# Optimization experiments

Hardware: AMD Instinct MI355X
Metric: run time of the kernel (lower is better)

Reference implementation:

```python
import jax, jax.numpy as jnp
import numpy as np

N, E = 20000, 160000          # nodes, edges
D, ED, H, NH = 32, 16, 64, 4  # node_dim, edge_dim, hidden_dim, num_heads
G, MAXN = 100, 200            # graphs, nodes per graph (equal-size graphs)
HD = H // NH                  # head dim


def setup_inputs() -> dict:
    key = jax.random.key(0)
    ks = jax.random.split(key, 20)
    p = lambda k, shp: jax.random.normal(k, shp, dtype=jnp.float32) * 0.05
    return {
        "x": jax.random.normal(ks[0], (N, D), dtype=jnp.float32),
        "edge_index": jax.random.randint(ks[1], (2, E), 0, N),
        "edge_attr": jax.random.normal(ks[2], (E, ED), dtype=jnp.float32),
        "batch": jnp.arange(N, dtype=jnp.int32) // MAXN,  # 100 graphs x 200 nodes
        "en_w1": p(ks[3], (H, ED)), "en_b1": p(ks[4], (H,)),
        "en_w2": p(ks[5], (D * H, H)), "en_b2": p(ks[6], (D * H,)),
        "root_w": p(ks[7], (D, H)), "conv_b": p(ks[8], (H,)),
        "in_proj_w": p(ks[9], (3 * H, H)), "in_proj_b": p(ks[10], (3 * H,)),
        "out_proj_w": p(ks[11], (H, H)), "out_proj_b": p(ks[12], (H,)),
        "lin1_w": p(ks[13], (H, H)), "lin1_b": p(ks[14], (H,)),
        "lin2_w": p(ks[15], (1, H)), "lin2_b": p(ks[16], (1,)),
    }


def reference(x, edge_index, edge_attr, batch,
              en_w1, en_b1, en_w2, en_b2, root_w, conv_b,
              in_proj_w, in_proj_b, out_proj_w, out_proj_b,
              lin1_w, lin1_b, lin2_w, lin2_b):
    src, dst = edge_index[0], edge_index[1]
    # ---- NNConv: edge MLP -> per-edge weight [E, D, H], gather-matmul-scatter-mean ----
    h = jax.nn.relu(edge_attr @ en_w1.T + en_b1)
    w_e = (h @ en_w2.T + en_b2).reshape(E, D, H)
    msgs = jnp.einsum('ed,edh->eh', x[src], w_e)                 # [E, H]
    agg = jax.ops.segment_sum(msgs, dst, num_segments=N)         # scatter-sum by dest
    cnt = jax.ops.segment_sum(jnp.ones((E,), x.dtype), dst, num_segments=N)
    agg = agg / jnp.maximum(cnt, 1.0)[:, None]                   # mean aggregation
    xh = jax.nn.relu(agg + x @ root_w + conv_b)                  # root weight + bias
    # ---- to_dense_batch (batch is sorted) ----
    counts = jax.ops.segment_sum(jnp.ones((N,), jnp.int32), batch, num_segments=G)
    starts = jnp.concatenate([jnp.zeros((1,), jnp.int32), jnp.cumsum(counts)[:-1]])
    pos = jnp.arange(N, dtype=jnp.int32) - starts[batch]
    dense = jnp.zeros((G, MAXN, H), xh.dtype).at[batch, pos].set(xh)
    mask = jnp.zeros((G, MAXN), bool).at[batch, pos].set(True)
    # ---- MultiheadAttention (self-attn, key_padding_mask = ~mask) ----
    qkv = dense @ in_proj_w.T + in_proj_b                        # [G, MAXN, 3H]
    q, k, v = jnp.split(qkv, 3, axis=-1)
    sh = lambda t: t.reshape(G, MAXN, NH, HD).transpose(0, 2, 1, 3)  # [G, NH, MAXN, HD]
    q, k, v = sh(q), sh(k), sh(v)
    scores = jnp.einsum('gnqd,gnkd->gnqk', q, k) / jnp.sqrt(jnp.float32(HD))
    scores = jnp.where(mask[:, None, None, :], scores, jnp.float32(-1e9))
    attn = jax.nn.softmax(scores, axis=-1)
    ctx = jnp.einsum('gnqk,gnkd->gnqd', attn, v)
    ctx = ctx.transpose(0, 2, 1, 3).reshape(G, MAXN, H)
    attn_out = ctx @ out_proj_w.T + out_proj_b
    # zero out padded positions, masked mean pool
    attn_out = jnp.where(mask[:, :, None], attn_out, 0.0)
    graph_emb = attn_out.sum(axis=1) / mask.sum(axis=1, keepdims=True).astype(attn_out.dtype)
    h1 = jax.nn.relu(graph_emb @ lin1_w.T + lin1_b)
    return (h1 @ lin2_w.T + lin2_b).squeeze(1)                   # [G]
```

## Files before the change

kernel.cpp:

```cpp
#include <hip/hip_runtime.h>
#include <math.h>

#define N_N 20000
#define N_E 160000
#define KA 2112
#define NKB 66

typedef __attribute__((ext_vector_type(8))) short bfrag;
typedef __attribute__((ext_vector_type(4))) float facc;

__device__ __forceinline__ unsigned short f2bf(float f) {
  union { float f; unsigned u; } v; v.f = f;
  unsigned u = v.u;
  return (unsigned short)((u + 0x7FFF + ((u >> 16) & 1)) >> 16);
}
__device__ __forceinline__ unsigned pk2(float a, float b) {
  return (unsigned)f2bf(a) | ((unsigned)f2bf(b) << 16);
}
__device__ __forceinline__ float bflo(unsigned u) {
  union { unsigned u; float f; } v; v.u = u << 16; return v.f;
}
__device__ __forceinline__ float bfhi(unsigned u) {
  union { unsigned u; float f; } v; v.u = u & 0xffff0000u; return v.f;
}
__device__ __forceinline__ void gload16(const void* g, void* s) {
  __builtin_amdgcn_global_load_lds(
      (const __attribute__((address_space(1))) void*)g,
      (__attribute__((address_space(3))) void*)s, 16, 0, 0);
}

__global__ __launch_bounds__(256) void k_mlp1(const float* __restrict__ ea,
    const float* __restrict__ w1, const float* __restrict__ b1,
    const int* __restrict__ elist, unsigned short* __restrict__ hes) {
  int t = threadIdx.x, w = t >> 6, j = t & 63;
  int p0 = blockIdx.x * 32 + w * 8;
  float wr[16];
#pragma unroll
  for (int i = 0; i < 16; ++i) wr[i] = w1[j * 16 + i];
  float bj = b1[j];
#pragma unroll
  for (int q = 0; q < 8; ++q) {
    int p = p0 + q;
    int e = elist[p];
    const float* a = ea + (size_t)e * 16;
    float s = bj;
#pragma unroll
    for (int i = 0; i < 16; ++i) s += a[i] * wr[i];
    hes[(size_t)p * 64 + j] = f2bf(fmaxf(s, 0.f));
  }
}

__global__ __launch_bounds__(256) void k_hist(const int* __restrict__ eidx,
    int* __restrict__ cnt) {
  int e = blockIdx.x * 256 + threadIdx.x;
  atomicAdd(&cnt[eidx[N_E + e]], 1);
}

__global__ __launch_bounds__(1024) void k_scan(int* __restrict__ hist,
    int* __restrict__ starts) {
  __shared__ int part[1024];
  int t = threadIdx.x;
  const int CH = 20;
  int lo = t * CH;
  int hi = lo + CH; if (hi > N_N) hi = N_N;
  int s = 0;
  for (int i = lo; i < hi; ++i) s += hist[i];
  part[t] = s;
  __syncthreads();
  for (int off = 1; off < 1024; off <<= 1) {
    int v = (t >= off) ? part[t - off] : 0;
    __syncthreads();
    part[t] += v;
    __syncthreads();
  }
  int run = (t == 0) ? 0 : part[t - 1];
  for (int i = lo; i < hi; ++i) {
    int h = hist[i];
    starts[i] = run;
    hist[i] = run;
    run += h;
  }
  if (t == 1023) starts[N_N] = part[1023];
}

__global__ __launch_bounds__(256) void k_scatter(const int* __restrict__ eidx,
    int* __restrict__ cur, int* __restrict__ elist, int* __restrict__ srcl) {
  int e = blockIdx.x * 256 + threadIdx.x;
  int dn = eidx[N_E + e];
  int pos = atomicAdd(&cur[dn], 1);
  elist[pos] = e;
  srcl[pos] = eidx[e];
}

__global__ __launch_bounds__(256) void k_pack(const float* __restrict__ w2,
    const float* __restrict__ b2f, const float* __restrict__ rootw,
    const float* __restrict__ inw,
    unsigned short* __restrict__ Bp, unsigned short* __restrict__ B2p,
    int* __restrict__ cursor, float* __restrict__ pool) {
  int idx = blockIdx.x * 256 + threadIdx.x;
  const int GT = 580 * 256;
  if (idx < 135168) {
    int i = idx & 7, l = (idx >> 3) & 63, cbkb = idx >> 9;
    int cb = cbkb & 3, kb = cbkb >> 2;
    int r = kb * 32 + ((l >> 4) << 3) + i;
    int c = (cb << 4) + (l & 15);
    float v;
    if (r < 2048) { int d = r >> 6, k = r & 63; v = w2[((d << 6) + c) * 64 + k]; }
    else if (r < 2080) v = b2f[((r - 2048) << 6) + c];
    else v = rootw[((r - 2080) << 6) + c];
    Bp[idx] = f2bf(v);
  } else if (idx < 135168 + 12288) {
    int k2 = idx - 135168;
    int i = k2 & 7, l = (k2 >> 3) & 63, cbkb = k2 >> 9;
    int cb = cbkb % 12, kb = cbkb / 12;
    int r = kb * 32 + ((l >> 4) << 3) + i;
    int c = (cb << 4) + (l & 15);
    B2p[k2] = f2bf(inw[c * 64 + r]);
  }
  for (int i = idx; i < N_N; i += GT) cursor[i] = 0;
  for (int i = idx; i < 6400; i += GT) pool[i] = 0.f;
}

#define FMA8(hv, base, xv) \
  acc[base + 0] += xv * bflo(hv.x); acc[base + 1] += xv * bfhi(hv.x); \
  acc[base + 2] += xv * bflo(hv.y); acc[base + 3] += xv * bfhi(hv.y); \
  acc[base + 4] += xv * bflo(hv.z); acc[base + 5] += xv * bfhi(hv.z); \
  acc[base + 6] += xv * bflo(hv.w); acc[base + 7] += xv * bfhi(hv.w);

__global__ __launch_bounds__(512, 4) void k_fused(const float* __restrict__ x,
    const unsigned short* __restrict__ hes, const int* __restrict__ starts,
    const int* __restrict__ srcl,
    const unsigned short* __restrict__ Bp, const unsigned short* __restrict__ B2p,
    const float* __restrict__ convb, const float* __restrict__ inb,
    float* __restrict__ Qb, float* __restrict__ Kb, float* __restrict__ Vb) {
  __shared__ unsigned short Ps[8 * KA];
  __shared__ __align__(16) unsigned short Hs[8 * 512];
  __shared__ __align__(16) float Xs[8 * 256];
  __shared__ unsigned short xhT[8 * 68];
  int t = threadIdx.x, w = t >> 6, l = t & 63;
  int n0 = blockIdx.x * 8;
  int d0 = l >> 3, l31 = l & 31;
  unsigned short* Hw = Hs + w * 512;
  float* Xw = Xs + w * 256;
  {
    int n = n0 + w;
    int s0 = starts[n], s1 = starts[n + 1];
    float acc[32];
#pragma unroll
    for (int z = 0; z < 32; ++z) acc[z] = 0.f;
    float xs = 0.f;
#pragma unroll 1
    for (int c0 = s0; c0 < s1; c0 += 64) {
      int srv = 0;
      if (c0 + l < s1) srv = srcl[c0 + l];
      int cc = s1 - c0; if (cc > 64) cc = 64;
#pragma unroll 1
      for (int j0 = 0; j0 < cc; j0 += 8) {
        int nedge = cc - j0; if (nedge > 8) nedge = 8;
        int slot = c0 + j0 + (l >> 3); if (slot >= s1) slot = s1 - 1;
        gload16(hes + (size_t)slot * 64 + (l & 7) * 8, Hw);
        int sr = __shfl(srv, j0 + (l >> 3));
        gload16(x + (size_t)sr * 32 + (l & 7) * 4, Xw);
        asm volatile("s_waitcnt vmcnt(0)" ::: "memory");
#pragma unroll 1
        for (int i = 0; i < nedge; i += 2) {
          uint4 hA = *(const uint4*)(Hw + i * 64 + (l & 7) * 8);
          float a0 = Xw[i * 32 + d0],      a1 = Xw[i * 32 + d0 + 8];
          float a2 = Xw[i * 32 + d0 + 16], a3 = Xw[i * 32 + d0 + 24];
          float xsa = Xw[i * 32 + l31];
          uint4 hB = {0, 0, 0, 0};
          float b0 = 0.f, b1 = 0.f, b2 = 0.f, b3 = 0.f, xsb = 0.f;
          if (i + 1 < nedge) {
            hB = *(const uint4*)(Hw + (i + 1) * 64 + (l & 7) * 8);
            b0 = Xw[(i + 1) * 32 + d0];      b1 = Xw[(i + 1) * 32 + d0 + 8];
            b2 = Xw[(i + 1) * 32 + d0 + 16]; b3 = Xw[(i + 1) * 32 + d0 + 24];
            xsb = Xw[(i + 1) * 32 + l31];
          }
          FMA8(hA, 0, a0) FMA8(hA, 8, a1) FMA8(hA, 16, a2) FMA8(hA, 24, a3)
          FMA8(hB, 0, b0) FMA8(hB, 8, b1) FMA8(hB, 16, b2) FMA8(hB, 24, b3)
          xs += xsa + xsb;
        }
      }
    }
    int s = w;
#pragma unroll
    for (int q = 0; q < 4; ++q) {
      int scr = (l + 64 * q) ^ s;
      uint4 o;
      o.x = pk2(acc[q * 8 + 0], acc[q * 8 + 1]);
      o.y = pk2(acc[q * 8 + 2], acc[q * 8 + 3]);
      o.z = pk2(acc[q * 8 + 4], acc[q * 8 + 5]);
      o.w = pk2(acc[q * 8 + 6], acc[q * 8 + 7]);
      *(uint4*)(Ps + w * KA + scr * 8) = o;
    }
    if (l < 32) {
      int cnt = s1 - s0; if (cnt < 1) cnt = 1;
      int c1 = (256 + (l >> 3)) ^ s, c2 = (260 + (l >> 3)) ^ s;
      Ps[w * KA + c1 * 8 + (l & 7)] = f2bf(xs);
      Ps[w * KA + c2 * 8 + (l & 7)] = f2bf(x[(size_t)n * 32 + l] * (float)cnt);
    }
  }
  __syncthreads();
  int col = l & 15, sub = l >> 4;
  int arow = col & 7;
  if (w < 4) {
    const bfrag* Bb = (const bfrag*)Bp + w * 64 + l;
    facc ac = {0.f, 0.f, 0.f, 0.f};
#pragma unroll 4
    for (int kb = 0; kb < NKB; ++kb) {
      int scr = ((kb << 2) + sub) ^ arow;
      bfrag af = *(const bfrag*)(Ps + arow * KA + scr * 8);
      ac = __builtin_amdgcn_mfma_f32_16x16x32_bf16(af, Bb[kb * 256], ac, 0, 0, 0);
    }
    float cv = convb[w * 16 + col];
#pragma unroll
    for (int j = 0; j < 4; ++j) {
      int m = sub * 4 + j;
      if (m < 8) {
        int n = n0 + m;
        int cnt = starts[n + 1] - starts[n]; if (cnt < 1) cnt = 1;
        float inv = 1.f / (float)cnt;
        xhT[m * 68 + w * 16 + col] = f2bf(fmaxf(ac[j] * inv + cv, 0.f));
      }
    }
  }
  __syncthreads();
  if (w < 4) {
    bfrag af0 = *(const bfrag*)&xhT[(col & 7) * 68 + sub * 8];
    bfrag af1 = *(const bfrag*)&xhT[(col & 7) * 68 + 32 + sub * 8];
    const bfrag* B2b = (const bfrag*)B2p + l;
#pragma unroll
    for (int c3 = 0; c3 < 3; ++c3) {
      int cb = w * 3 + c3;
      facc qa = {0.f, 0.f, 0.f, 0.f};
      qa = __builtin_amdgcn_mfma_f32_16x16x32_bf16(af0, B2b[cb * 64], qa, 0, 0, 0);
      qa = __builtin_amdgcn_mfma_f32_16x16x32_bf16(af1, B2b[(12 + cb) * 64], qa, 0, 0, 0);
#pragma unroll
      for (int j = 0; j < 4; ++j) {
        int m = sub * 4 + j;
        if (m < 8) {
          int n = n0 + m;
          int g = n / 200, p = n - g * 200;
          int c = cb * 16 + col;
          float v = qa[j] + inb[c];
          int part = c >> 6, rem = c & 63, hh = rem >> 4, dd = rem & 15;
          float* dst = (part == 0) ? Qb : (part == 1 ? Kb : Vb);
          dst[(((size_t)g * 4 + hh) * 200 + p) * 16 + dd] = v;
        }
      }
    }
  }
}

__global__ __launch_bounds__(256) void k_attn(const float* __restrict__ Qb,
    const float* __restrict__ Kb, const float* __restrict__ Vb,
    float* __restrict__ pool) {
  __shared__ unsigned short Ks[224 * 24];
  __shared__ unsigned short Vt[16 * 232];
  __shared__ unsigned short Pl[4][16 * 40];
  __shared__ float pw[4][16];
  int t = threadIdx.x;
  int gh = blockIdx.x >> 1, half = blockIdx.x & 1;
  size_t base = (size_t)gh * 3200;
  for (int idx = t; idx < 224 * 16; idx += 256) {
    int row = idx >> 4, d = idx & 15;
    float kv = (row < 200) ? Kb[base + idx] : 0.f;
    float vv = (row < 200) ? Vb[base + idx] : 0.f;
    Ks[row * 24 + d] = f2bf(kv);
    Vt[d * 232 + row] = f2bf(vv);
  }
  __syncthreads();
  int w = t >> 6, l = t & 63;
  int sub = l >> 4, col = l & 15;
  int qlo = half * 7, qhi = half ? 13 : 7;
  float pacc = 0.f;
  for (int qt = qlo + w; qt < qhi; qt += 4) {
    bfrag qf = {0, 0, 0, 0, 0, 0, 0, 0};
    int q = qt * 16 + col;
    if (sub < 2 && q < 200) {
      const float* qp = Qb + base + q * 16 + sub * 8;
      float4 qa = *(const float4*)qp;
      float4 qb = *(const float4*)(qp + 4);
      qf[0] = (short)f2bf(qa.x); qf[1] = (short)f2bf(qa.y);
      qf[2] = (short)f2bf(qa.z); qf[3] = (short)f2bf(qa.w);
      qf[4] = (short)f2bf(qb.x); qf[5] = (short)f2bf(qb.y);
      qf[6] = (short)f2bf(qb.z); qf[7] = (short)f2bf(qb.w);
    }
    facc o = {0.f, 0.f, 0.f, 0.f};
    float srow0 = 0.f, srow1 = 0.f, srow2 = 0.f, srow3 = 0.f;
    for (int kt2 = 0; kt2 < 7; ++kt2) {
      int kt0 = kt2 * 2, kt1 = kt0 + 1;
      bfrag kf0 = {0, 0, 0, 0, 0, 0, 0, 0};
      bfrag kf1 = {0, 0, 0, 0, 0, 0, 0, 0};
      if (sub < 2) {
        kf0 = *(const bfrag*)&Ks[(kt0 * 16 + col) * 24 + sub * 8];
        kf1 = *(const bfrag*)&Ks[(kt1 * 16 + col) * 24 + sub * 8];
      }
      facc z = {0.f, 0.f, 0.f, 0.f};
      facc s0 = __builtin_amdgcn_mfma_f32_16x16x32_bf16(qf, kf0, z, 0, 0, 0);
      facc s1 = __builtin_amdgcn_mfma_f32_16x16x32_bf16(qf, kf1, z, 0, 0, 0);
      bool ok0 = (kt0 * 16 + col) < 200;
      bool ok1 = (kt1 * 16 + col) < 200;
#pragma unroll
      for (int j = 0; j < 4; ++j) {
        float e0 = ok0 ? __expf(s0[j] * 0.25f) : 0.f;
        float e1 = ok1 ? __expf(s1[j] * 0.25f) : 0.f;
        if (j == 0) { srow0 += e0 + e1; } else if (j == 1) { srow1 += e0 + e1; }
        else if (j == 2) { srow2 += e0 + e1; } else { srow3 += e0 + e1; }
        int qr = (sub << 2) + j;
        Pl[w][qr * 40 + col] = f2bf(e0);
        Pl[w][qr * 40 + 16 + col] = f2bf(e1);
      }
      bfrag pf = *(const bfrag*)&Pl[w][col * 40 + sub * 8];
      bfrag vf = *(const bfrag*)&Vt[col * 232 + kt2 * 32 + sub * 8];
      o = __builtin_amdgcn_mfma_f32_16x16x32_bf16(pf, vf, o, 0, 0, 0);
    }
#pragma unroll
    for (int off = 1; off < 16; off <<= 1) {
      srow0 += __shfl_xor(srow0, off);
      srow1 += __shfl_xor(srow1, off);
      srow2 += __shfl_xor(srow2, off);
      srow3 += __shfl_xor(srow3, off);
    }
#pragma unroll
    for (int j = 0; j < 4; ++j) {
      int qq = qt * 16 + (sub << 2) + j;
      float sr = (j == 0) ? srow0 : (j == 1) ? srow1 : (j == 2) ? srow2 : srow3;
      if (qq < 200) pacc += o[j] / sr;
    }
  }
  pacc += __shfl_xor(pacc, 16);
  pacc += __shfl_xor(pacc, 32);
  if (l < 16) pw[w][l] = pacc;
  __syncthreads();
  if (t < 16) {
    float v = pw[0][t] + pw[1][t] + pw[2][t] + pw[3][t];
    atomicAdd(&pool[gh * 16 + t], v);
  }
}

__global__ __launch_bounds__(64) void k_head(const float* __restrict__ pool,
    const float* __restrict__ ow, const float* __restrict__ ob,
    const float* __restrict__ w1, const float* __restrict__ b1,
    const float* __restrict__ w2, const float* __restrict__ b2,
    float* __restrict__ out) {
  __shared__ float ms[64], es[64];
  int g = blockIdx.x, t = threadIdx.x;
  ms[t] = pool[g * 64 + t] * (1.f / 200.f);
  __syncthreads();
  float e = ob[t];
  for (int j = 0; j < 64; ++j) e += ow[t * 64 + j] * ms[j];
  es[t] = e;
  __syncthreads();
  float h1 = b1[t];
  for (int j = 0; j < 64; ++j) h1 += w1[t * 64 + j] * es[j];
  h1 = fmaxf(h1, 0.f);
  float pr = h1 * w2[t];
  for (int off = 32; off >= 1; off >>= 1) pr += __shfl_xor(pr, off);
  if (t == 0) out[g] = pr + b2[0];
}

extern "C" void kernel_launch(void* const* d_in, const int* in_sizes, int n_in,
                              void* d_out, int out_size, void* d_ws, size_t ws_size,
                              hipStream_t stream) {
  (void)in_sizes; (void)n_in;
  const float* x      = (const float*)d_in[0];
  const int*   eidx   = (const int*)d_in[1];
  const float* ea     = (const float*)d_in[2];
  const float* en_w1  = (const float*)d_in[4];
  const float* en_b1  = (const float*)d_in[5];
  const float* en_w2  = (const float*)d_in[6];
  const float* en_b2  = (const float*)d_in[7];
  const float* root_w = (const float*)d_in[8];
  const float* conv_b = (const float*)d_in[9];
  const float* in_w   = (const float*)d_in[10];
  const float* in_b   = (const float*)d_in[11];
  const float* out_w  = (const float*)d_in[12];
  const float* out_b  = (const float*)d_in[13];
  const float* l1w    = (const float*)d_in[14];
  const float* l1b    = (const float*)d_in[15];
  const float* l2w    = (const float*)d_in[16];
  const float* l2b    = (const float*)d_in[17];
  float* out = (float*)d_out;

  char* w = (char*)d_ws;
  unsigned short* hes = (unsigned short*)w;
  float* Qb  = (float*)(w + 20480000);
  float* Kb  = (float*)(w + 25600000);
  float* Vb  = (float*)(w + 30720000);
  float* pool = (float*)(w + 35840000);
  char* r3 = w + 35870000;
  unsigned short* Bp  = (unsigned short*)r3;
  unsigned short* B2p = (unsigned short*)(r3 + 270336);
  int* starts = (int*)(r3 + 270336 + 24576);
  int* elist  = starts + (N_N + 4);
  int* srcl   = elist + N_E;
  int* cursor = srcl + N_E;
  size_t need = 35870000 + 270336 + 24576
              + (size_t)(N_N + 4) * 4 + 2 * (size_t)N_E * 4 + (size_t)N_N * 4;
  if (ws_size < need || out_size < 100) return;

  k_pack<<<580, 256, 0, stream>>>(en_w2, en_b2, root_w, in_w, Bp, B2p, cursor, pool);
  k_hist<<<N_E / 256, 256, 0, stream>>>(eidx, cursor);
  k_scan<<<1, 1024, 0, stream>>>(cursor, starts);
  k_scatter<<<N_E / 256, 256, 0, stream>>>(eidx, cursor, elist, srcl);
  k_mlp1<<<5000, 256, 0, stream>>>(ea, en_w1, en_b1, elist, hes);
  k_fused<<<2500, 512, 0, stream>>>(x, hes, starts, srcl, Bp, B2p,
                                    conv_b, in_b, Qb, Kb, Vb);
  k_attn<<<800, 256, 0, stream>>>(Qb, Kb, Vb, pool);
  k_head<<<100, 64, 0, stream>>>(pool, out_w, out_b, l1w, l1b, l2w, l2b, out);
}
```

Baseline: 165.3 us.

## Fuse edge MLP into message kernel, merge histogram into pack, fold head into attention

The first edge-MLP layer (edge_attr -> 64 hidden ReLU) moves into the fused message kernel. Each wave loads raw 16-float edge attributes and computes the bf16 hidden activations in LDS, so the 20 MB intermediate no longer makes a global round trip. The destination histogram now runs inside the weight-packing kernel, with a memset zeroing the cursor first. The final MLP head is folded into the attention kernel through a last-block-done atomic counter per graph. Together these remove three launches at the cost of some extra ALU work per edge chunk and a serialized tail in the last block for each graph.

```diff
diff --git a/kernel.cpp b/kernel.cpp
--- a/kernel.cpp
+++ b/kernel.cpp
@@ -29,76 +29,12 @@
       (__attribute__((address_space(3))) void*)s, 16, 0, 0);
 }
 
-__global__ __launch_bounds__(256) void k_mlp1(const float* __restrict__ ea,
-    const float* __restrict__ w1, const float* __restrict__ b1,
-    const int* __restrict__ elist, unsigned short* __restrict__ hes) {
-  int t = threadIdx.x, w = t >> 6, j = t & 63;
-  int p0 = blockIdx.x * 32 + w * 8;
-  float wr[16];
-#pragma unroll
-  for (int i = 0; i < 16; ++i) wr[i] = w1[j * 16 + i];
-  float bj = b1[j];
-#pragma unroll
-  for (int q = 0; q < 8; ++q) {
-    int p = p0 + q;
-    int e = elist[p];
-    const float* a = ea + (size_t)e * 16;
-    float s = bj;
-#pragma unroll
-    for (int i = 0; i < 16; ++i) s += a[i] * wr[i];
-    hes[(size_t)p * 64 + j] = f2bf(fmaxf(s, 0.f));
-  }
-}
-
-__global__ __launch_bounds__(256) void k_hist(const int* __restrict__ eidx,
-    int* __restrict__ cnt) {
-  int e = blockIdx.x * 256 + threadIdx.x;
-  atomicAdd(&cnt[eidx[N_E + e]], 1);
-}
-
-__global__ __launch_bounds__(1024) void k_scan(int* __restrict__ hist,
-    int* __restrict__ starts) {
-  __shared__ int part[1024];
-  int t = threadIdx.x;
-  const int CH = 20;
-  int lo = t * CH;
-  int hi = lo + CH; if (hi > N_N) hi = N_N;
-  int s = 0;
-  for (int i = lo; i < hi; ++i) s += hist[i];
-  part[t] = s;
-  __syncthreads();
-  for (int off = 1; off < 1024; off <<= 1) {
-    int v = (t >= off) ? part[t - off] : 0;
-    __syncthreads();
-    part[t] += v;
-    __syncthreads();
-  }
-  int run = (t == 0) ? 0 : part[t - 1];
-  for (int i = lo; i < hi; ++i) {
-    int h = hist[i];
-    starts[i] = run;
-    hist[i] = run;
-    run += h;
-  }
-  if (t == 1023) starts[N_N] = part[1023];
-}
-
-__global__ __launch_bounds__(256) void k_scatter(const int* __restrict__ eidx,
-    int* __restrict__ cur, int* __restrict__ elist, int* __restrict__ srcl) {
-  int e = blockIdx.x * 256 + threadIdx.x;
-  int dn = eidx[N_E + e];
-  int pos = atomicAdd(&cur[dn], 1);
-  elist[pos] = e;
-  srcl[pos] = eidx[e];
-}
-
-__global__ __launch_bounds__(256) void k_pack(const float* __restrict__ w2,
+__global__ __launch_bounds__(256) void k_packhist(const float* __restrict__ w2,
     const float* __restrict__ b2f, const float* __restrict__ rootw,
-    const float* __restrict__ inw,
+    const float* __restrict__ inw, const int* __restrict__ eidx,
     unsigned short* __restrict__ Bp, unsigned short* __restrict__ B2p,
-    int* __restrict__ cursor, float* __restrict__ pool) {
+    int* __restrict__ cursor, float* __restrict__ pool, int* __restrict__ gcnt) {
   int idx = blockIdx.x * 256 + threadIdx.x;
-  const int GT = 580 * 256;
   if (idx < 135168) {
     int i = idx & 7, l = (idx >> 3) & 63, cbkb = idx >> 9;
     int cb = cbkb & 3, kb = cbkb >> 2;
@@ -117,8 +53,45 @@
     int c = (cb << 4) + (l & 15);
     B2p[k2] = f2bf(inw[c * 64 + r]);
   }
-  for (int i = idx; i < N_N; i += GT) cursor[i] = 0;
-  for (int i = idx; i < 6400; i += GT) pool[i] = 0.f;
+  if (idx < N_E) atomicAdd(&cursor[eidx[N_E + idx]], 1);
+  if (idx < 6400) pool[idx] = 0.f;
+  if (idx < 100) gcnt[idx] = 0;
+}
+
+__global__ __launch_bounds__(1024) void k_scan(int* __restrict__ hist,
+    int* __restrict__ starts) {
+  __shared__ int part[1024];
+  int t = threadIdx.x;
+  const int CH = 20;
+  int lo = t * CH;
+  int hi = lo + CH; if (hi > N_N) hi = N_N;
+  int s = 0;
+  for (int i = lo; i < hi; ++i) s += hist[i];
+  part[t] = s;
+  __syncthreads();
+  for (int off = 1; off < 1024; off <<= 1) {
+    int v = (t >= off) ? part[t - off] : 0;
+    __syncthreads();
+    part[t] += v;
+    __syncthreads();
+  }
+  int run = (t == 0) ? 0 : part[t - 1];
+  for (int i = lo; i < hi; ++i) {
+    int h = hist[i];
+    starts[i] = run;
+    hist[i] = run;
+    run += h;
+  }
+  if (t == 1023) starts[N_N] = part[1023];
+}
+
+__global__ __launch_bounds__(256) void k_scatter(const int* __restrict__ eidx,
+    int* __restrict__ cur, int* __restrict__ elist, int* __restrict__ srcl) {
+  int e = blockIdx.x * 256 + threadIdx.x;
+  int dn = eidx[N_E + e];
+  int pos = atomicAdd(&cur[dn], 1);
+  elist[pos] = e;
+  srcl[pos] = eidx[e];
 }
 
 #define FMA8(hv, base, xv) \
@@ -128,20 +101,28 @@
   acc[base + 6] += xv * bflo(hv.w); acc[base + 7] += xv * bfhi(hv.w);
 
 __global__ __launch_bounds__(512, 4) void k_fused(const float* __restrict__ x,
-    const unsigned short* __restrict__ hes, const int* __restrict__ starts,
-    const int* __restrict__ srcl,
+    const float* __restrict__ ea, const float* __restrict__ w1,
+    const float* __restrict__ b1, const int* __restrict__ starts,
+    const int* __restrict__ elist, const int* __restrict__ srcl,
     const unsigned short* __restrict__ Bp, const unsigned short* __restrict__ B2p,
     const float* __restrict__ convb, const float* __restrict__ inb,
     float* __restrict__ Qb, float* __restrict__ Kb, float* __restrict__ Vb) {
   __shared__ unsigned short Ps[8 * KA];
-  __shared__ __align__(16) unsigned short Hs[8 * 512];
+  __shared__ __align__(16) float EaS[8 * 128];
   __shared__ __align__(16) float Xs[8 * 256];
+  __shared__ unsigned short HeS[8 * 512];
   __shared__ unsigned short xhT[8 * 68];
   int t = threadIdx.x, w = t >> 6, l = t & 63;
   int n0 = blockIdx.x * 8;
   int d0 = l >> 3, l31 = l & 31;
-  unsigned short* Hw = Hs + w * 512;
-  float* Xw = Xs + w * 256;
+  float* EaW = EaS + w * 128;
+  float* XwW = Xs + w * 256;
+  unsigned short* HeW = HeS + w * 512;
+  float w1r[16];
+#pragma unroll
+  for (int i = 0; i < 4; ++i)
+    *(float4*)&w1r[i * 4] = *(const float4*)(w1 + l * 16 + i * 4);
+  float b1l = b1[l];
   {
     int n = n0 + w;
     int s0 = starts[n], s1 = starts[n + 1];
@@ -151,33 +132,46 @@
     float xs = 0.f;
 #pragma unroll 1
     for (int c0 = s0; c0 < s1; c0 += 64) {
-      int srv = 0;
-      if (c0 + l < s1) srv = srcl[c0 + l];
+      int eev = 0, srv = 0;
+      if (c0 + l < s1) { eev = elist[c0 + l]; srv = srcl[c0 + l]; }
       int cc = s1 - c0; if (cc > 64) cc = 64;
 #pragma unroll 1
       for (int j0 = 0; j0 < cc; j0 += 8) {
         int nedge = cc - j0; if (nedge > 8) nedge = 8;
-        int slot = c0 + j0 + (l >> 3); if (slot >= s1) slot = s1 - 1;
-        gload16(hes + (size_t)slot * 64 + (l & 7) * 8, Hw);
+        int esrc = __shfl(eev, j0 + (l >> 2));
+        if (l < 32) gload16(ea + (size_t)esrc * 16 + (l & 3) * 4, EaW);
         int sr = __shfl(srv, j0 + (l >> 3));
-        gload16(x + (size_t)sr * 32 + (l & 7) * 4, Xw);
+        gload16(x + (size_t)sr * 32 + (l & 7) * 4, XwW);
         asm volatile("s_waitcnt vmcnt(0)" ::: "memory");
+#pragma unroll
+        for (int e = 0; e < 8; ++e) {
+          float4 q0 = ((const float4*)EaW)[e * 4 + 0];
+          float4 q1 = ((const float4*)EaW)[e * 4 + 1];
+          float4 q2 = ((const float4*)EaW)[e * 4 + 2];
+          float4 q3 = ((const float4*)EaW)[e * 4 + 3];
+          float h = b1l;
+          h += q0.x * w1r[0] + q0.y * w1r[1] + q0.z * w1r[2] + q0.w * w1r[3];
+          h += q1.x * w1r[4] + q1.y * w1r[5] + q1.z * w1r[6] + q1.w * w1r[7];
+          h += q2.x * w1r[8] + q2.y * w1r[9] + q2.z * w1r[10] + q2.w * w1r[11];
+          h += q3.x * w1r[12] + q3.y * w1r[13] + q3.z * w1r[14] + q3.w * w1r[15];
+          HeW[e * 64 + l] = f2bf(fmaxf(h, 0.f));
+        }
 #pragma unroll 1
         for (int i = 0; i < nedge; i += 2) {
-          uint4 hA = *(const uint4*)(Hw + i * 64 + (l & 7) * 8);
-          float a0 = Xw[i * 32 + d0],      a1 = Xw[i * 32 + d0 + 8];
-          float a2 = Xw[i * 32 + d0 + 16], a3 = Xw[i * 32 + d0 + 24];
-          float xsa = Xw[i * 32 + l31];
+          uint4 hA = *(const uint4*)(HeW + i * 64 + (l & 7) * 8);
+          float a0 = XwW[i * 32 + d0],      a1 = XwW[i * 32 + d0 + 8];
+          float a2 = XwW[i * 32 + d0 + 16], a3 = XwW[i * 32 + d0 + 24];
+          float xsa = XwW[i * 32 + l31];
           uint4 hB = {0, 0, 0, 0};
-          float b0 = 0.f, b1 = 0.f, b2 = 0.f, b3 = 0.f, xsb = 0.f;
+          float b0 = 0.f, b1f = 0.f, b2 = 0.f, b3 = 0.f, xsb = 0.f;
           if (i + 1 < nedge) {
-            hB = *(const uint4*)(Hw + (i + 1) * 64 + (l & 7) * 8);
-            b0 = Xw[(i + 1) * 32 + d0];      b1 = Xw[(i + 1) * 32 + d0 + 8];
-            b2 = Xw[(i + 1) * 32 + d0 + 16]; b3 = Xw[(i + 1) * 32 + d0 + 24];
-            xsb = Xw[(i + 1) * 32 + l31];
+            hB = *(const uint4*)(HeW + (i + 1) * 64 + (l & 7) * 8);
+            b0 = XwW[(i + 1) * 32 + d0];      b1f = XwW[(i + 1) * 32 + d0 + 8];
+            b2 = XwW[(i + 1) * 32 + d0 + 16]; b3 = XwW[(i + 1) * 32 + d0 + 24];
+            xsb = XwW[(i + 1) * 32 + l31];
           }
           FMA8(hA, 0, a0) FMA8(hA, 8, a1) FMA8(hA, 16, a2) FMA8(hA, 24, a3)
-          FMA8(hB, 0, b0) FMA8(hB, 8, b1) FMA8(hB, 16, b2) FMA8(hB, 24, b3)
+          FMA8(hB, 0, b0) FMA8(hB, 8, b1f) FMA8(hB, 16, b2) FMA8(hB, 24, b3)
           xs += xsa + xsb;
         }
       }
@@ -254,11 +248,17 @@
 
 __global__ __launch_bounds__(256) void k_attn(const float* __restrict__ Qb,
     const float* __restrict__ Kb, const float* __restrict__ Vb,
-    float* __restrict__ pool) {
+    float* __restrict__ pool, int* __restrict__ gcnt,
+    const float* __restrict__ ow, const float* __restrict__ ob,
+    const float* __restrict__ w1, const float* __restrict__ b1,
+    const float* __restrict__ w2, const float* __restrict__ b2,
+    float* __restrict__ out) {
   __shared__ unsigned short Ks[224 * 24];
   __shared__ unsigned short Vt[16 * 232];
   __shared__ unsigned short Pl[4][16 * 40];
   __shared__ float pw[4][16];
+  __shared__ float ms[64], es[64];
+  __shared__ int lastflag;
   int t = threadIdx.x;
   int gh = blockIdx.x >> 1, half = blockIdx.x & 1;
   size_t base = (size_t)gh * 3200;
@@ -333,31 +333,38 @@
   pacc += __shfl_xor(pacc, 32);
   if (l < 16) pw[w][l] = pacc;
   __syncthreads();
+  int g = gh >> 2;
   if (t < 16) {
     float v = pw[0][t] + pw[1][t] + pw[2][t] + pw[3][t];
     atomicAdd(&pool[gh * 16 + t], v);
   }
-}
-
-__global__ __launch_bounds__(64) void k_head(const float* __restrict__ pool,
-    const float* __restrict__ ow, const float* __restrict__ ob,
-    const float* __restrict__ w1, const float* __restrict__ b1,
-    const float* __restrict__ w2, const float* __restrict__ b2,
-    float* __restrict__ out) {
-  __shared__ float ms[64], es[64];
-  int g = blockIdx.x, t = threadIdx.x;
-  ms[t] = pool[g * 64 + t] * (1.f / 200.f);
-  __syncthreads();
-  float e = ob[t];
-  for (int j = 0; j < 64; ++j) e += ow[t * 64 + j] * ms[j];
-  es[t] = e;
-  __syncthreads();
-  float h1 = b1[t];
-  for (int j = 0; j < 64; ++j) h1 += w1[t * 64 + j] * es[j];
-  h1 = fmaxf(h1, 0.f);
-  float pr = h1 * w2[t];
-  for (int off = 32; off >= 1; off >>= 1) pr += __shfl_xor(pr, off);
-  if (t == 0) out[g] = pr + b2[0];
+  if (t == 0) {
+    __threadfence();
+    int done = atomicAdd(&gcnt[g], 1);
+    lastflag = (done == 7) ? 1 : 0;
+  }
+  __syncthreads();
+  if (lastflag) {
+    if (t < 64) {
+      float v = atomicAdd(&pool[g * 64 + t], 0.f);
+      ms[t] = v * (1.f / 200.f);
+    }
+    __syncthreads();
+    if (t < 64) {
+      float e = ob[t];
+      for (int j = 0; j < 64; ++j) e += ow[t * 64 + j] * ms[j];
+      es[t] = e;
+    }
+    __syncthreads();
+    if (t < 64) {
+      float h1 = b1[t];
+      for (int j = 0; j < 64; ++j) h1 += w1[t * 64 + j] * es[j];
+      h1 = fmaxf(h1, 0.f);
+      float pr = h1 * w2[t];
+      for (int off = 32; off >= 1; off >>= 1) pr += __shfl_xor(pr, off);
+      if (t == 0) out[g] = pr + b2[0];
+    }
+  }
 }
 
 extern "C" void kernel_launch(void* const* d_in, const int* in_sizes, int n_in,
@@ -384,29 +391,29 @@
   float* out = (float*)d_out;
 
   char* w = (char*)d_ws;
-  unsigned short* hes = (unsigned short*)w;
-  float* Qb  = (float*)(w + 20480000);
-  float* Kb  = (float*)(w + 25600000);
-  float* Vb  = (float*)(w + 30720000);
-  float* pool = (float*)(w + 35840000);
-  char* r3 = w + 35870000;
+  float* Qb  = (float*)w;
+  float* Kb  = (float*)(w + 5120000);
+  float* Vb  = (float*)(w + 10240000);
+  float* pool = (float*)(w + 15360000);
+  int* gcnt  = (int*)(w + 15385600);
+  char* r3 = w + 15386112;
   unsigned short* Bp  = (unsigned short*)r3;
   unsigned short* B2p = (unsigned short*)(r3 + 270336);
   int* starts = (int*)(r3 + 270336 + 24576);
   int* elist  = starts + (N_N + 4);
   int* srcl   = elist + N_E;
   int* cursor = srcl + N_E;
-  size_t need = 35870000 + 270336 + 24576
+  size_t need = 15386112 + 270336 + 24576
               + (size_t)(N_N + 4) * 4 + 2 * (size_t)N_E * 4 + (size_t)N_N * 4;
   if (ws_size < need || out_size < 100) return;
 
-  k_pack<<<580, 256, 0, stream>>>(en_w2, en_b2, root_w, in_w, Bp, B2p, cursor, pool);
-  k_hist<<<N_E / 256, 256, 0, stream>>>(eidx, cursor);
+  hipMemsetAsync(cursor, 0, N_N * 4, stream);
+  k_packhist<<<625, 256, 0, stream>>>(en_w2, en_b2, root_w, in_w, eidx,
+                                      Bp, B2p, cursor, pool, gcnt);
   k_scan<<<1, 1024, 0, stream>>>(cursor, starts);
   k_scatter<<<N_E / 256, 256, 0, stream>>>(eidx, cursor, elist, srcl);
-  k_mlp1<<<5000, 256, 0, stream>>>(ea, en_w1, en_b1, elist, hes);
-  k_fused<<<2500, 512, 0, stream>>>(x, hes, starts, srcl, Bp, B2p,
-                                    conv_b, in_b, Qb, Kb, Vb);
-  k_attn<<<800, 256, 0, stream>>>(Qb, Kb, Vb, pool);
-  k_head<<<100, 64, 0, stream>>>(pool, out_w, out_b, l1w, l1b, l2w, l2b, out);
-}
+  k_fused<<<2500, 512, 0, stream>>>(x, ea, en_w1, en_b1, starts, elist, srcl,
+                                    Bp, B2p, conv_b, in_b, Qb, Kb, Vb);
+  k_attn<<<800, 256, 0, stream>>>(Qb, Kb, Vb, pool, gcnt,
+                                  out_w, out_b, l1w, l1b, l2w, l2b, out);
+}
```

Result: no change. 167.6 us (+1.4%).

## Fuse histogram into pack, head into attention, and block-cooperative edge staging

Applied to the files above, without the earlier changes.

Merges the degree histogram into the weight-packing kernel (zeroing the cursor with a memset), and folds the final head MLP into the attention kernel: the last block per graph, found through an atomic counter, computes the output. In the fused NNConv kernel, all 8 waves of a block now cooperatively stage up to 96 contiguous edges' hidden features and source x rows into shared memory, then each wave consumes its own node's range. This removes two kernel launches and balances edge loading across waves when node degrees are skewed. In exchange it adds block-wide barriers per chunk, extra LDS, and threadfence/atomic overhead in attention.

```diff
diff --git a/kernel.cpp b/kernel.cpp
--- a/kernel.cpp
+++ b/kernel.cpp
@@ -50,55 +50,12 @@
   }
 }
 
-__global__ __launch_bounds__(256) void k_hist(const int* __restrict__ eidx,
-    int* __restrict__ cnt) {
-  int e = blockIdx.x * 256 + threadIdx.x;
-  atomicAdd(&cnt[eidx[N_E + e]], 1);
-}
-
-__global__ __launch_bounds__(1024) void k_scan(int* __restrict__ hist,
-    int* __restrict__ starts) {
-  __shared__ int part[1024];
-  int t = threadIdx.x;
-  const int CH = 20;
-  int lo = t * CH;
-  int hi = lo + CH; if (hi > N_N) hi = N_N;
-  int s = 0;
-  for (int i = lo; i < hi; ++i) s += hist[i];
-  part[t] = s;
-  __syncthreads();
-  for (int off = 1; off < 1024; off <<= 1) {
-    int v = (t >= off) ? part[t - off] : 0;
-    __syncthreads();
-    part[t] += v;
-    __syncthreads();
-  }
-  int run = (t == 0) ? 0 : part[t - 1];
-  for (int i = lo; i < hi; ++i) {
-    int h = hist[i];
-    starts[i] = run;
-    hist[i] = run;
-    run += h;
-  }
-  if (t == 1023) starts[N_N] = part[1023];
-}
-
-__global__ __launch_bounds__(256) void k_scatter(const int* __restrict__ eidx,
-    int* __restrict__ cur, int* __restrict__ elist, int* __restrict__ srcl) {
-  int e = blockIdx.x * 256 + threadIdx.x;
-  int dn = eidx[N_E + e];
-  int pos = atomicAdd(&cur[dn], 1);
-  elist[pos] = e;
-  srcl[pos] = eidx[e];
-}
-
-__global__ __launch_bounds__(256) void k_pack(const float* __restrict__ w2,
+__global__ __launch_bounds__(256) void k_packhist(const float* __restrict__ w2,
     const float* __restrict__ b2f, const float* __restrict__ rootw,
-    const float* __restrict__ inw,
+    const float* __restrict__ inw, const int* __restrict__ eidx,
     unsigned short* __restrict__ Bp, unsigned short* __restrict__ B2p,
-    int* __restrict__ cursor, float* __restrict__ pool) {
+    int* __restrict__ cursor, float* __restrict__ pool, int* __restrict__ gcnt) {
   int idx = blockIdx.x * 256 + threadIdx.x;
-  const int GT = 580 * 256;
   if (idx < 135168) {
     int i = idx & 7, l = (idx >> 3) & 63, cbkb = idx >> 9;
     int cb = cbkb & 3, kb = cbkb >> 2;
@@ -117,8 +74,45 @@
     int c = (cb << 4) + (l & 15);
     B2p[k2] = f2bf(inw[c * 64 + r]);
   }
-  for (int i = idx; i < N_N; i += GT) cursor[i] = 0;
-  for (int i = idx; i < 6400; i += GT) pool[i] = 0.f;
+  if (idx < N_E) atomicAdd(&cursor[eidx[N_E + idx]], 1);
+  if (idx < 6400) pool[idx] = 0.f;
+  if (idx < 100) gcnt[idx] = 0;
+}
+
+__global__ __launch_bounds__(1024) void k_scan(int* __restrict__ hist,
+    int* __restrict__ starts) {
+  __shared__ int part[1024];
+  int t = threadIdx.x;
+  const int CH = 20;
+  int lo = t * CH;
+  int hi = lo + CH; if (hi > N_N) hi = N_N;
+  int s = 0;
+  for (int i = lo; i < hi; ++i) s += hist[i];
+  part[t] = s;
+  __syncthreads();
+  for (int off = 1; off < 1024; off <<= 1) {
+    int v = (t >= off) ? part[t - off] : 0;
+    __syncthreads();
+    part[t] += v;
+    __syncthreads();
+  }
+  int run = (t == 0) ? 0 : part[t - 1];
+  for (int i = lo; i < hi; ++i) {
+    int h = hist[i];
+    starts[i] = run;
+    hist[i] = run;
+    run += h;
+  }
+  if (t == 1023) starts[N_N] = part[1023];
+}
+
+__global__ __launch_bounds__(256) void k_scatter(const int* __restrict__ eidx,
+    int* __restrict__ cur, int* __restrict__ elist, int* __restrict__ srcl) {
+  int e = blockIdx.x * 256 + threadIdx.x;
+  int dn = eidx[N_E + e];
+  int pos = atomicAdd(&cur[dn], 1);
+  elist[pos] = e;
+  srcl[pos] = eidx[e];
 }
 
 #define FMA8(hv, base, xv) \
@@ -134,53 +128,57 @@
     const float* __restrict__ convb, const float* __restrict__ inb,
     float* __restrict__ Qb, float* __restrict__ Kb, float* __restrict__ Vb) {
   __shared__ unsigned short Ps[8 * KA];
-  __shared__ __align__(16) unsigned short Hs[8 * 512];
-  __shared__ __align__(16) float Xs[8 * 256];
+  __shared__ __align__(16) unsigned short HeSt[96 * 64];
+  __shared__ __align__(16) float XSt[96 * 32];
   __shared__ unsigned short xhT[8 * 68];
   int t = threadIdx.x, w = t >> 6, l = t & 63;
   int n0 = blockIdx.x * 8;
   int d0 = l >> 3, l31 = l & 31;
-  unsigned short* Hw = Hs + w * 512;
-  float* Xw = Xs + w * 256;
   {
     int n = n0 + w;
-    int s0 = starts[n], s1 = starts[n + 1];
+    int s0n = starts[n], s1n = starts[n + 1];
+    int S0 = starts[n0], S1 = starts[n0 + 8];
     float acc[32];
 #pragma unroll
     for (int z = 0; z < 32; ++z) acc[z] = 0.f;
     float xs = 0.f;
 #pragma unroll 1
-    for (int c0 = s0; c0 < s1; c0 += 64) {
-      int srv = 0;
-      if (c0 + l < s1) srv = srcl[c0 + l];
-      int cc = s1 - c0; if (cc > 64) cc = 64;
+    for (int c0 = S0; c0 < S1; c0 += 96) {
+      int L = S1 - c0; if (L > 96) L = 96;
+      int nsl = (L + 7) >> 3;
 #pragma unroll 1
-      for (int j0 = 0; j0 < cc; j0 += 8) {
-        int nedge = cc - j0; if (nedge > 8) nedge = 8;
-        int slot = c0 + j0 + (l >> 3); if (slot >= s1) slot = s1 - 1;
-        gload16(hes + (size_t)slot * 64 + (l & 7) * 8, Hw);
-        int sr = __shfl(srv, j0 + (l >> 3));
-        gload16(x + (size_t)sr * 32 + (l & 7) * 4, Xw);
-        asm volatile("s_waitcnt vmcnt(0)" ::: "memory");
+      for (int sl = w; sl < nsl; sl += 8) {
+        int base = c0 + sl * 8;
+        int slot = base + (l >> 3); if (slot >= S1) slot = S1 - 1;
+        gload16(hes + (size_t)slot * 64 + (l & 7) * 8, HeSt + sl * 512);
+        int sr = srcl[slot];
+        gload16(x + (size_t)sr * 32 + (l & 7) * 4, XSt + sl * 256);
+      }
+      asm volatile("s_waitcnt vmcnt(0)" ::: "memory");
+      __syncthreads();
+      int lo = s0n > c0 ? s0n : c0;
+      int hi = s1n < c0 + 96 ? s1n : c0 + 96;
 #pragma unroll 1
-        for (int i = 0; i < nedge; i += 2) {
-          uint4 hA = *(const uint4*)(Hw + i * 64 + (l & 7) * 8);
-          float a0 = Xw[i * 32 + d0],      a1 = Xw[i * 32 + d0 + 8];
-          float a2 = Xw[i * 32 + d0 + 16], a3 = Xw[i * 32 + d0 + 24];
-          float xsa = Xw[i * 32 + l31];
-          uint4 hB = {0, 0, 0, 0};
-          float b0 = 0.f, b1 = 0.f, b2 = 0.f, b3 = 0.f, xsb = 0.f;
-          if (i + 1 < nedge) {
-            hB = *(const uint4*)(Hw + (i + 1) * 64 + (l & 7) * 8);
-            b0 = Xw[(i + 1) * 32 + d0];      b1 = Xw[(i + 1) * 32 + d0 + 8];
-            b2 = Xw[(i + 1) * 32 + d0 + 16]; b3 = Xw[(i + 1) * 32 + d0 + 24];
-            xsb = Xw[(i + 1) * 32 + l31];
-          }
-          FMA8(hA, 0, a0) FMA8(hA, 8, a1) FMA8(hA, 16, a2) FMA8(hA, 24, a3)
-          FMA8(hB, 0, b0) FMA8(hB, 8, b1) FMA8(hB, 16, b2) FMA8(hB, 24, b3)
-          xs += xsa + xsb;
+      for (int i = lo; i < hi; i += 2) {
+        int idx = i - c0;
+        uint4 hA = *(const uint4*)(HeSt + idx * 64 + (l & 7) * 8);
+        float a0 = XSt[idx * 32 + d0],      a1 = XSt[idx * 32 + d0 + 8];
+        float a2 = XSt[idx * 32 + d0 + 16], a3 = XSt[idx * 32 + d0 + 24];
+        float xsa = XSt[idx * 32 + l31];
+        uint4 hB = {0, 0, 0, 0};
+        float b0 = 0.f, b1 = 0.f, b2 = 0.f, b3 = 0.f, xsb = 0.f;
+        if (i + 1 < hi) {
+          int idx2 = idx + 1;
+          hB = *(const uint4*)(HeSt + idx2 * 64 + (l & 7) * 8);
+          b0 = XSt[idx2 * 32 + d0];      b1 = XSt[idx2 * 32 + d0 + 8];
+          b2 = XSt[idx2 * 32 + d0 + 16]; b3 = XSt[idx2 * 32 + d0 + 24];
+          xsb = XSt[idx2 * 32 + l31];
         }
-      }
+        FMA8(hA, 0, a0) FMA8(hA, 8, a1) FMA8(hA, 16, a2) FMA8(hA, 24, a3)
+        FMA8(hB, 0, b0) FMA8(hB, 8, b1) FMA8(hB, 16, b2) FMA8(hB, 24, b3)
+        xs += xsa + xsb;
+      }
+      __syncthreads();
     }
     int s = w;
 #pragma unroll
@@ -194,7 +192,7 @@
       *(uint4*)(Ps + w * KA + scr * 8) = o;
     }
     if (l < 32) {
-      int cnt = s1 - s0; if (cnt < 1) cnt = 1;
+      int cnt = s1n - s0n; if (cnt < 1) cnt = 1;
       int c1 = (256 + (l >> 3)) ^ s, c2 = (260 + (l >> 3)) ^ s;
       Ps[w * KA + c1 * 8 + (l & 7)] = f2bf(xs);
       Ps[w * KA + c2 * 8 + (l & 7)] = f2bf(x[(size_t)n * 32 + l] * (float)cnt);
@@ -254,11 +252,17 @@
 
 __global__ __launch_bounds__(256) void k_attn(const float* __restrict__ Qb,
     const float* __restrict__ Kb, const float* __restrict__ Vb,
-    float* __restrict__ pool) {
+    float* __restrict__ pool, int* __restrict__ gcnt,
+    const float* __restrict__ ow, const float* __restrict__ ob,
+    const float* __restrict__ w1, const float* __restrict__ b1,
+    const float* __restrict__ w2, const float* __restrict__ b2,
+    float* __restrict__ out) {
   __shared__ unsigned short Ks[224 * 24];
   __shared__ unsigned short Vt[16 * 232];
   __shared__ unsigned short Pl[4][16 * 40];
   __shared__ float pw[4][16];
+  __shared__ float ms[64], es[64];
+  __shared__ int lastflag;
   int t = threadIdx.x;
   int gh = blockIdx.x >> 1, half = blockIdx.x & 1;
   size_t base = (size_t)gh * 3200;
@@ -333,31 +337,38 @@
   pacc += __shfl_xor(pacc, 32);
   if (l < 16) pw[w][l] = pacc;
   __syncthreads();
+  int g = gh >> 2;
   if (t < 16) {
     float v = pw[0][t] + pw[1][t] + pw[2][t] + pw[3][t];
     atomicAdd(&pool[gh * 16 + t], v);
   }
-}
-
-__global__ __launch_bounds__(64) void k_head(const float* __restrict__ pool,
-    const float* __restrict__ ow, const float* __restrict__ ob,
-    const float* __restrict__ w1, const float* __restrict__ b1,
-    const float* __restrict__ w2, const float* __restrict__ b2,
-    float* __restrict__ out) {
-  __shared__ float ms[64], es[64];
-  int g = blockIdx.x, t = threadIdx.x;
-  ms[t] = pool[g * 64 + t] * (1.f / 200.f);
-  __syncthreads();
-  float e = ob[t];
-  for (int j = 0; j < 64; ++j) e += ow[t * 64 + j] * ms[j];
-  es[t] = e;
-  __syncthreads();
-  float h1 = b1[t];
-  for (int j = 0; j < 64; ++j) h1 += w1[t * 64 + j] * es[j];
-  h1 = fmaxf(h1, 0.f);
-  float pr = h1 * w2[t];
-  for (int off = 32; off >= 1; off >>= 1) pr += __shfl_xor(pr, off);
-  if (t == 0) out[g] = pr + b2[0];
+  if (t == 0) {
+    __threadfence();
+    int done = atomicAdd(&gcnt[g], 1);
+    lastflag = (done == 7) ? 1 : 0;
+  }
+  __syncthreads();
+  if (lastflag) {
+    if (t < 64) {
+      float v = atomicAdd(&pool[g * 64 + t], 0.f);
+      ms[t] = v * (1.f / 200.f);
+    }
+    __syncthreads();
+    if (t < 64) {
+      float e = ob[t];
+      for (int j = 0; j < 64; ++j) e += ow[t * 64 + j] * ms[j];
+      es[t] = e;
+    }
+    __syncthreads();
+    if (t < 64) {
+      float h1 = b1[t];
+      for (int j = 0; j < 64; ++j) h1 += w1[t * 64 + j] * es[j];
+      h1 = fmaxf(h1, 0.f);
+      float pr = h1 * w2[t];
+      for (int off = 32; off >= 1; off >>= 1) pr += __shfl_xor(pr, off);
+      if (t == 0) out[g] = pr + b2[0];
+    }
+  }
 }
 
 extern "C" void kernel_launch(void* const* d_in, const int* in_sizes, int n_in,
@@ -389,24 +400,26 @@
   float* Kb  = (float*)(w + 25600000);
   float* Vb  = (float*)(w + 30720000);
   float* pool = (float*)(w + 35840000);
-  char* r3 = w + 35870000;
+  int* gcnt  = (int*)(w + 35865600);
+  char* r3 = w + 35866112;
   unsigned short* Bp  = (unsigned short*)r3;
   unsigned short* B2p = (unsigned short*)(r3 + 270336);
   int* starts = (int*)(r3 + 270336 + 24576);
   int* elist  = starts + (N_N + 4);
   int* srcl   = elist + N_E;
   int* cursor = srcl + N_E;
-  size_t need = 35870000 + 270336 + 24576
+  size_t need = 35866112 + 270336 + 24576
               + (size_t)(N_N + 4) * 4 + 2 * (size_t)N_E * 4 + (size_t)N_N * 4;
   if (ws_size < need || out_size < 100) return;
 
-  k_pack<<<580, 256, 0, stream>>>(en_w2, en_b2, root_w, in_w, Bp, B2p, cursor, pool);
-  k_hist<<<N_E / 256, 256, 0, stream>>>(eidx, cursor);
+  hipMemsetAsync(cursor, 0, N_N * 4, stream);
+  k_packhist<<<625, 256, 0, stream>>>(en_w2, en_b2, root_w, in_w, eidx,
+                                      Bp, B2p, cursor, pool, gcnt);
   k_scan<<<1, 1024, 0, stream>>>(cursor, starts);
   k_scatter<<<N_E / 256, 256, 0, stream>>>(eidx, cursor, elist, srcl);
   k_mlp1<<<5000, 256, 0, stream>>>(ea, en_w1, en_b1, elist, hes);
   k_fused<<<2500, 512, 0, stream>>>(x, hes, starts, srcl, Bp, B2p,
                                     conv_b, in_b, Qb, Kb, Vb);
-  k_attn<<<800, 256, 0, stream>>>(Qb, Kb, Vb, pool);
-  k_head<<<100, 64, 0, stream>>>(pool, out_w, out_b, l1w, l1b, l2w, l2b, out);
-}
+  k_attn<<<800, 256, 0, stream>>>(Qb, Kb, Vb, pool, gcnt,
+                                  out_w, out_b, l1w, l1b, l2w, l2b, out);
+}
```

New measurement: 184.4 us. +11.5%, slower.

## Fuse histogram into pack, scatter into edge MLP, and head into attention

Applied to the files above, without the earlier changes.

Folds the dest histogram into the weight-packing kernel and zeroes the cursor with a memset. Merges the CSR scatter with the first edge-MLP layer so the hidden activations are written straight to their sorted slot, which removes the elist buffer and one kernel. Fuses the readout head into the attention kernel using a per-graph completion counter so the last block finishes the graph. Together these cut three launches and one intermediate pass, at the cost of threadfence/atomic ordering complexity.

```diff
diff --git a/kernel.cpp b/kernel.cpp
--- a/kernel.cpp
+++ b/kernel.cpp
@@ -29,76 +29,12 @@
       (__attribute__((address_space(3))) void*)s, 16, 0, 0);
 }
 
-__global__ __launch_bounds__(256) void k_mlp1(const float* __restrict__ ea,
-    const float* __restrict__ w1, const float* __restrict__ b1,
-    const int* __restrict__ elist, unsigned short* __restrict__ hes) {
-  int t = threadIdx.x, w = t >> 6, j = t & 63;
-  int p0 = blockIdx.x * 32 + w * 8;
-  float wr[16];
-#pragma unroll
-  for (int i = 0; i < 16; ++i) wr[i] = w1[j * 16 + i];
-  float bj = b1[j];
-#pragma unroll
-  for (int q = 0; q < 8; ++q) {
-    int p = p0 + q;
-    int e = elist[p];
-    const float* a = ea + (size_t)e * 16;
-    float s = bj;
-#pragma unroll
-    for (int i = 0; i < 16; ++i) s += a[i] * wr[i];
-    hes[(size_t)p * 64 + j] = f2bf(fmaxf(s, 0.f));
-  }
-}
-
-__global__ __launch_bounds__(256) void k_hist(const int* __restrict__ eidx,
-    int* __restrict__ cnt) {
-  int e = blockIdx.x * 256 + threadIdx.x;
-  atomicAdd(&cnt[eidx[N_E + e]], 1);
-}
-
-__global__ __launch_bounds__(1024) void k_scan(int* __restrict__ hist,
-    int* __restrict__ starts) {
-  __shared__ int part[1024];
-  int t = threadIdx.x;
-  const int CH = 20;
-  int lo = t * CH;
-  int hi = lo + CH; if (hi > N_N) hi = N_N;
-  int s = 0;
-  for (int i = lo; i < hi; ++i) s += hist[i];
-  part[t] = s;
-  __syncthreads();
-  for (int off = 1; off < 1024; off <<= 1) {
-    int v = (t >= off) ? part[t - off] : 0;
-    __syncthreads();
-    part[t] += v;
-    __syncthreads();
-  }
-  int run = (t == 0) ? 0 : part[t - 1];
-  for (int i = lo; i < hi; ++i) {
-    int h = hist[i];
-    starts[i] = run;
-    hist[i] = run;
-    run += h;
-  }
-  if (t == 1023) starts[N_N] = part[1023];
-}
-
-__global__ __launch_bounds__(256) void k_scatter(const int* __restrict__ eidx,
-    int* __restrict__ cur, int* __restrict__ elist, int* __restrict__ srcl) {
-  int e = blockIdx.x * 256 + threadIdx.x;
-  int dn = eidx[N_E + e];
-  int pos = atomicAdd(&cur[dn], 1);
-  elist[pos] = e;
-  srcl[pos] = eidx[e];
-}
-
-__global__ __launch_bounds__(256) void k_pack(const float* __restrict__ w2,
+__global__ __launch_bounds__(256) void k_packhist(const float* __restrict__ w2,
     const float* __restrict__ b2f, const float* __restrict__ rootw,
-    const float* __restrict__ inw,
+    const float* __restrict__ inw, const int* __restrict__ eidx,
     unsigned short* __restrict__ Bp, unsigned short* __restrict__ B2p,
-    int* __restrict__ cursor, float* __restrict__ pool) {
+    int* __restrict__ cursor, float* __restrict__ pool, int* __restrict__ gcnt) {
   int idx = blockIdx.x * 256 + threadIdx.x;
-  const int GT = 580 * 256;
   if (idx < 135168) {
     int i = idx & 7, l = (idx >> 3) & 63, cbkb = idx >> 9;
     int cb = cbkb & 3, kb = cbkb >> 2;
@@ -117,8 +53,66 @@
     int c = (cb << 4) + (l & 15);
     B2p[k2] = f2bf(inw[c * 64 + r]);
   }
-  for (int i = idx; i < N_N; i += GT) cursor[i] = 0;
-  for (int i = idx; i < 6400; i += GT) pool[i] = 0.f;
+  if (idx < N_E) atomicAdd(&cursor[eidx[N_E + idx]], 1);
+  if (idx < 6400) pool[idx] = 0.f;
+  if (idx < 100) gcnt[idx] = 0;
+}
+
+__global__ __launch_bounds__(1024) void k_scan(int* __restrict__ hist,
+    int* __restrict__ starts) {
+  __shared__ int part[1024];
+  int t = threadIdx.x;
+  const int CH = 20;
+  int lo = t * CH;
+  int hi = lo + CH; if (hi > N_N) hi = N_N;
+  int s = 0;
+  for (int i = lo; i < hi; ++i) s += hist[i];
+  part[t] = s;
+  __syncthreads();
+  for (int off = 1; off < 1024; off <<= 1) {
+    int v = (t >= off) ? part[t - off] : 0;
+    __syncthreads();
+    part[t] += v;
+    __syncthreads();
+  }
+  int run = (t == 0) ? 0 : part[t - 1];
+  for (int i = lo; i < hi; ++i) {
+    int h = hist[i];
+    starts[i] = run;
+    hist[i] = run;
+    run += h;
+  }
+  if (t == 1023) starts[N_N] = part[1023];
+}
+
+__global__ __launch_bounds__(256) void k_scatmlp(const int* __restrict__ eidx,
+    const float* __restrict__ ea, const float* __restrict__ w1,
+    const float* __restrict__ b1, int* __restrict__ cur,
+    int* __restrict__ srcl, unsigned short* __restrict__ hes) {
+  int t = threadIdx.x, w = t >> 6, l = t & 63;
+  int e0 = blockIdx.x * 32 + w * 8;
+  float wr[16];
+#pragma unroll
+  for (int i = 0; i < 4; ++i)
+    *(float4*)&wr[i * 4] = *(const float4*)(w1 + l * 16 + i * 4);
+  float bl = b1[l];
+  int pos = 0;
+  if (l < 8) {
+    int e = e0 + l;
+    int dn = eidx[N_E + e];
+    pos = atomicAdd(&cur[dn], 1);
+    srcl[pos] = eidx[e];
+  }
+#pragma unroll
+  for (int q = 0; q < 8; ++q) {
+    int e = e0 + q;
+    const float* a = ea + (size_t)e * 16;
+    float s = bl;
+#pragma unroll
+    for (int i = 0; i < 16; ++i) s += a[i] * wr[i];
+    int p = __shfl(pos, q);
+    hes[(size_t)p * 64 + l] = f2bf(fmaxf(s, 0.f));
+  }
 }
 
 #define FMA8(hv, base, xv) \
@@ -254,11 +248,17 @@
 
 __global__ __launch_bounds__(256) void k_attn(const float* __restrict__ Qb,
     const float* __restrict__ Kb, const float* __restrict__ Vb,
-    float* __restrict__ pool) {
+    float* __restrict__ pool, int* __restrict__ gcnt,
+    const float* __restrict__ ow, const float* __restrict__ ob,
+    const float* __restrict__ w1, const float* __restrict__ b1,
+    const float* __restrict__ w2, const float* __restrict__ b2,
+    float* __restrict__ out) {
   __shared__ unsigned short Ks[224 * 24];
   __shared__ unsigned short Vt[16 * 232];
   __shared__ unsigned short Pl[4][16 * 40];
   __shared__ float pw[4][16];
+  __shared__ float ms[64], es[64];
+  __shared__ int lastflag;
   int t = threadIdx.x;
   int gh = blockIdx.x >> 1, half = blockIdx.x & 1;
   size_t base = (size_t)gh * 3200;
@@ -333,31 +333,38 @@
   pacc += __shfl_xor(pacc, 32);
   if (l < 16) pw[w][l] = pacc;
   __syncthreads();
+  int g = gh >> 2;
   if (t < 16) {
     float v = pw[0][t] + pw[1][t] + pw[2][t] + pw[3][t];
     atomicAdd(&pool[gh * 16 + t], v);
   }
-}
-
-__global__ __launch_bounds__(64) void k_head(const float* __restrict__ pool,
-    const float* __restrict__ ow, const float* __restrict__ ob,
-    const float* __restrict__ w1, const float* __restrict__ b1,
-    const float* __restrict__ w2, const float* __restrict__ b2,
-    float* __restrict__ out) {
-  __shared__ float ms[64], es[64];
-  int g = blockIdx.x, t = threadIdx.x;
-  ms[t] = pool[g * 64 + t] * (1.f / 200.f);
-  __syncthreads();
-  float e = ob[t];
-  for (int j = 0; j < 64; ++j) e += ow[t * 64 + j] * ms[j];
-  es[t] = e;
-  __syncthreads();
-  float h1 = b1[t];
-  for (int j = 0; j < 64; ++j) h1 += w1[t * 64 + j] * es[j];
-  h1 = fmaxf(h1, 0.f);
-  float pr = h1 * w2[t];
-  for (int off = 32; off >= 1; off >>= 1) pr += __shfl_xor(pr, off);
-  if (t == 0) out[g] = pr + b2[0];
+  if (t == 0) {
+    __threadfence();
+    int done = atomicAdd(&gcnt[g], 1);
+    lastflag = (done == 7) ? 1 : 0;
+  }
+  __syncthreads();
+  if (lastflag) {
+    if (t < 64) {
+      float v = atomicAdd(&pool[g * 64 + t], 0.f);
+      ms[t] = v * (1.f / 200.f);
+    }
+    __syncthreads();
+    if (t < 64) {
+      float e = ob[t];
+      for (int j = 0; j < 64; ++j) e += ow[t * 64 + j] * ms[j];
+      es[t] = e;
+    }
+    __syncthreads();
+    if (t < 64) {
+      float h1 = b1[t];
+      for (int j = 0; j < 64; ++j) h1 += w1[t * 64 + j] * es[j];
+      h1 = fmaxf(h1, 0.f);
+      float pr = h1 * w2[t];
+      for (int off = 32; off >= 1; off >>= 1) pr += __shfl_xor(pr, off);
+      if (t == 0) out[g] = pr + b2[0];
+    }
+  }
 }
 
 extern "C" void kernel_launch(void* const* d_in, const int* in_sizes, int n_in,
@@ -389,24 +396,24 @@
   float* Kb  = (float*)(w + 25600000);
   float* Vb  = (float*)(w + 30720000);
   float* pool = (float*)(w + 35840000);
-  char* r3 = w + 35870000;
+  int* gcnt  = (int*)(w + 35865600);
+  char* r3 = w + 35866112;
   unsigned short* Bp  = (unsigned short*)r3;
   unsigned short* B2p = (unsigned short*)(r3 + 270336);
   int* starts = (int*)(r3 + 270336 + 24576);
-  int* elist  = starts + (N_N + 4);
-  int* srcl   = elist + N_E;
+  int* srcl   = starts + (N_N + 4);
   int* cursor = srcl + N_E;
-  size_t need = 35870000 + 270336 + 24576
-              + (size_t)(N_N + 4) * 4 + 2 * (size_t)N_E * 4 + (size_t)N_N * 4;
+  size_t need = 35866112 + 270336 + 24576
+              + (size_t)(N_N + 4) * 4 + (size_t)N_E * 4 + (size_t)N_N * 4;
   if (ws_size < need || out_size < 100) return;
 
-  k_pack<<<580, 256, 0, stream>>>(en_w2, en_b2, root_w, in_w, Bp, B2p, cursor, pool);
-  k_hist<<<N_E / 256, 256, 0, stream>>>(eidx, cursor);
+  hipMemsetAsync(cursor, 0, N_N * 4, stream);
+  k_packhist<<<625, 256, 0, stream>>>(en_w2, en_b2, root_w, in_w, eidx,
+                                      Bp, B2p, cursor, pool, gcnt);
   k_scan<<<1, 1024, 0, stream>>>(cursor, starts);
-  k_scatter<<<N_E / 256, 256, 0, stream>>>(eidx, cursor, elist, srcl);
-  k_mlp1<<<5000, 256, 0, stream>>>(ea, en_w1, en_b1, elist, hes);
+  k_scatmlp<<<5000, 256, 0, stream>>>(eidx, ea, en_w1, en_b1, cursor, srcl, hes);
   k_fused<<<2500, 512, 0, stream>>>(x, hes, starts, srcl, Bp, B2p,
                                     conv_b, in_b, Qb, Kb, Vb);
-  k_attn<<<800, 256, 0, stream>>>(Qb, Kb, Vb, pool);
-  k_head<<<100, 64, 0, stream>>>(pool, out_w, out_b, l1w, l1b, l2w, l2b, out);
-}
+  k_attn<<<800, 256, 0, stream>>>(Qb, Kb, Vb, pool, gcnt,
+                                  out_w, out_b, l1w, l1b, l2w, l2b, out);
+}
```

Result: slower. 171.1 us (+3.5%).
